# Kernel optimization log

Measured on AMD Instinct MI355X. Metric: run time of the kernel, lower is better.

## Reference

```python
import jax, jax.numpy as jnp
import numpy as np
from jax import lax

T = 8192
D_MODEL = 768
D_RNN = 1024
KW = 4  # conv kernel width


def setup_inputs() -> dict:
    key = jax.random.key(0)
    ks = jax.random.split(key, 9)
    x = jax.random.normal(ks[0], (T, D_MODEL), jnp.float32)
    # equinox nn.Linear(in, out): weight [out, in], bias [out]
    w1 = jax.random.normal(ks[1], (2 * D_RNN, D_MODEL), jnp.float32) / np.sqrt(D_MODEL)
    b1 = jnp.zeros((2 * D_RNN,), jnp.float32)
    # nn.Conv1d(d_rnn, d_rnn, 4, use_bias=False): kernel [out_ch, in_ch, kw]
    conv_w = jax.random.normal(ks[2], (D_RNN, D_RNN, KW), jnp.float32) / np.sqrt(D_RNN * KW)
    w_rg = jax.random.normal(ks[3], (2 * D_RNN, D_RNN), jnp.float32) / np.sqrt(D_RNN)
    b_rg = jnp.zeros((2 * D_RNN,), jnp.float32)
    w_out = jax.random.normal(ks[4], (D_MODEL, D_RNN), jnp.float32) / np.sqrt(D_RNN)
    b_out = jnp.zeros((D_MODEL,), jnp.float32)
    # Lambda ~ U(inv_sigmoid(0.9)^{1/8}, inv_sigmoid(0.999)^{1/8}) as in __init__
    inv_sig = lambda p: np.log(1.0 / (1.0 - p))
    lower = np.power(inv_sig(0.9), 1.0 / 8.0)
    upper = np.power(inv_sig(0.999), 1.0 / 8.0)
    Lambda = jax.random.uniform(ks[5], (D_RNN,), jnp.float32, lower, upper)
    return {"x": x, "w1": w1, "b1": b1, "conv_w": conv_w, "w_rg": w_rg,
            "b_rg": b_rg, "w_out": w_out, "b_out": b_out, "Lambda": Lambda}


def _rglru_forward(x, w1, b1, conv_w, w_rg, b_rg, w_out, b_out, Lambda):
    # lin1 then split into gate branch (gelu) and recurrent branch
    h = x @ w1.T + b1                       # [T, 2*D_RNN]
    a_branch = jax.nn.gelu(h[:, :D_RNN])    # [T, D_RNN]
    b_branch = h[:, D_RNN:]                 # [T, D_RNN]
    # causal conv1d: lhs [N=1, C, T], rhs [O, I, KW], left pad 3
    bc = lax.conv_general_dilated(b_branch.T[None], conv_w, (1,), [(KW - 1, 0)])[0].T  # [T, D_RNN]
    # RG-LRU gating
    g = jax.nn.sigmoid(bc @ w_rg.T + b_rg)  # [T, 2*D_RNN]
    inp_gate = g[:, :D_RNN]
    rec_gate = g[:, D_RNN:]
    a_t = jnp.exp(-8.0 * jax.nn.softplus(Lambda)[None, :] * rec_gate)  # [T, D_RNN]
    gated_x = jnp.sqrt(1.0 - a_t ** 2) * inp_gate * bc

    def rec_step(state, xs):
        gx, av = xs
        hn = av * state + gx
        return hn, hn

    _, y = lax.scan(rec_step, jnp.zeros((D_RNN,), x.dtype), (gated_x, a_t))
    return (a_branch * y) @ w_out.T + b_out  # [T, D_MODEL]


def reference(x, w1, b1, conv_w, w_rg, b_rg, w_out, b_out, Lambda):
    return _rglru_forward(x, w1, b1, conv_w, w_rg, b_rg, w_out, b_out, Lambda)
```

## Files before the change

kernel.cpp:

```cpp
#include <hip/hip_runtime.h>
#include <hip/hip_bf16.h>
#include <stdint.h>


#define T_LEN 8192
#define DM 768
#define DR 1024
#define NC 128
#define CL 64

typedef __bf16 bf16x8 __attribute__((ext_vector_type(8)));
typedef float  f32x4  __attribute__((ext_vector_type(4)));

#define AS1 __attribute__((address_space(1)))
#define AS3 __attribute__((address_space(3)))

__device__ __forceinline__ void cp16_g2l(const void* g, void* l) {
    __builtin_amdgcn_global_load_lds((const AS1 void*)g, (AS3 void*)l, 16, 0, 0);
}

__device__ __forceinline__ float gelu_tanh(float x) {
    const float inner = 0.7978845608028654f * (x + 0.044715f * x * x * x);
    return 0.5f * x * (1.f + tanhf(inner));
}

template<int BN, int EPI>
__global__ __launch_bounds__(256)
void gemm_mfma(const __hip_bfloat16* __restrict__ A,
               const __hip_bfloat16* __restrict__ B,
               const float* __restrict__ bias,
               void* __restrict__ Cv,
               int K, int lda, int N,
               __hip_bfloat16* __restrict__ D2)
{
    constexpr int NI = BN / 32;
    __shared__ __bf16 As[128 * 64];
    __shared__ __bf16 Bs[BN * 64];

    const int tid  = threadIdx.x;
    const int lane = tid & 63;
    const int wave = tid >> 6;
    const size_t m0 = (size_t)blockIdx.x * 128;
    const int    n0 = blockIdx.y * BN;
    const int wm = (wave >> 1) * 64;
    const int wn = (wave & 1) * (BN / 2);

    f32x4 acc[4][NI];
#pragma unroll
    for (int i = 0; i < 4; ++i)
#pragma unroll
        for (int j = 0; j < NI; ++j)
            acc[i][j] = f32x4{0.f, 0.f, 0.f, 0.f};

    const int frow = lane & 15;
    const int fq   = lane >> 4;

    for (int k0 = 0; k0 < K; k0 += 64) {
        __syncthreads();
#pragma unroll
        for (int q = 0; q < 4; ++q) {
            const int lin = q * 256 + tid;
            const int rr  = lin >> 3;
            const int gc  = (lin & 7) ^ (rr & 7);
            cp16_g2l(A + (m0 + rr) * (size_t)lda + k0 + gc * 8, &As[lin * 8]);
        }
#pragma unroll
        for (int q = 0; q < NI; ++q) {
            const int lin = q * 256 + tid;
            const int rr  = lin >> 3;
            const int gc  = (lin & 7) ^ (rr & 7);
            cp16_g2l(B + (size_t)(n0 + rr) * K + k0 + gc * 8, &Bs[lin * 8]);
        }
        __syncthreads();

#pragma unroll
        for (int ks = 0; ks < 2; ++ks) {
            bf16x8 af[4], bfr[NI];
#pragma unroll
            for (int mi = 0; mi < 4; ++mi) {
                const int R = wm + mi * 16 + frow;
                af[mi] = *(const bf16x8*)&As[R * 64 + (((ks * 4 + fq) ^ (R & 7)) * 8)];
            }
#pragma unroll
            for (int ni = 0; ni < NI; ++ni) {
                const int R = wn + ni * 16 + frow;
                bfr[ni] = *(const bf16x8*)&Bs[R * 64 + (((ks * 4 + fq) ^ (R & 7)) * 8)];
            }
#pragma unroll
            for (int mi = 0; mi < 4; ++mi)
#pragma unroll
                for (int ni = 0; ni < NI; ++ni)
                    acc[mi][ni] = __builtin_amdgcn_mfma_f32_16x16x32_bf16(
                        af[mi], bfr[ni], acc[mi][ni], 0, 0, 0);
        }
    }

    const int er = fq * 4;
    const int ec = frow;
#pragma unroll
    for (int ni = 0; ni < NI; ++ni) {
        const int n = n0 + wn + ni * 16 + ec;
        const float bv = bias ? bias[n] : 0.f;
#pragma unroll
        for (int mi = 0; mi < 4; ++mi) {
#pragma unroll
            for (int r2 = 0; r2 < 4; ++r2) {
                const size_t m = m0 + wm + mi * 16 + er + r2;
                const float v = acc[mi][ni][r2] + bv;
                if (EPI == 0) {
                    ((float*)Cv)[m * (size_t)N + n] = v;
                } else if (EPI == 1) {
                    ((__hip_bfloat16*)Cv)[m * (size_t)N + n] = __float2bfloat16(v);
                } else {
                    if (n < 1024)
                        ((__hip_bfloat16*)Cv)[m * 1024 + n] = __float2bfloat16(gelu_tanh(v));
                    else
                        D2[(m + 3) * 1024 + (n - 1024)] = __float2bfloat16(v);
                }
            }
        }
    }
}

__global__ __launch_bounds__(256)
void conv_mfma(const __hip_bfloat16* __restrict__ bbp,
               const __hip_bfloat16* __restrict__ W,
               __hip_bfloat16* __restrict__ C)
{
    __shared__ __bf16 As[132 * 32];
    __shared__ __bf16 Bs[4 * 128 * 32];

    const int tid  = threadIdx.x;
    const int lane = tid & 63;
    const int wave = tid >> 6;
    const size_t m0 = (size_t)blockIdx.x * 128;
    const int    n0 = blockIdx.y * 128;
    const int wm = (wave >> 1) * 64;
    const int wn = (wave & 1) * 64;

    f32x4 acc[4][4];
#pragma unroll
    for (int i = 0; i < 4; ++i)
#pragma unroll
        for (int j = 0; j < 4; ++j)
            acc[i][j] = f32x4{0.f, 0.f, 0.f, 0.f};

    const int frow = lane & 15;
    const int fq   = lane >> 4;

    for (int kc = 0; kc < 1024; kc += 32) {
        __syncthreads();
#pragma unroll
        for (int q = 0; q < 2; ++q) {
            const int lin = q * 256 + tid;
            const int rr  = lin >> 2;
            const int gc  = (lin & 3) ^ ((rr >> 1) & 3);
            cp16_g2l(bbp + (m0 + rr) * 1024 + kc + gc * 8, &As[lin * 8]);
        }
        if (tid < 16) {
            const int lin = 512 + tid;
            const int rr  = lin >> 2;
            const int gc  = (lin & 3) ^ ((rr >> 1) & 3);
            cp16_g2l(bbp + (m0 + rr) * 1024 + kc + gc * 8, &As[lin * 8]);
        }
#pragma unroll
        for (int s = 0; s < 4; ++s)
#pragma unroll
            for (int q = 0; q < 2; ++q) {
                const int lin = q * 256 + tid;
                const int rr  = lin >> 2;
                const int gc  = (lin & 3) ^ ((rr >> 1) & 3);
                cp16_g2l(W + (size_t)(n0 + rr) * 4096 + s * 1024 + kc + gc * 8,
                         &Bs[s * 4096 + lin * 8]);
            }
        __syncthreads();

#pragma unroll
        for (int s = 0; s < 4; ++s) {
            bf16x8 af[4], bfr[4];
#pragma unroll
            for (int mi = 0; mi < 4; ++mi) {
                const int R = wm + mi * 16 + frow + s;
                af[mi] = *(const bf16x8*)&As[R * 32 + ((fq ^ ((R >> 1) & 3)) * 8)];
            }
#pragma unroll
            for (int ni = 0; ni < 4; ++ni) {
                const int R = wn + ni * 16 + frow;
                bfr[ni] = *(const bf16x8*)&Bs[s * 4096 + R * 32 + ((fq ^ ((R >> 1) & 3)) * 8)];
            }
#pragma unroll
            for (int mi = 0; mi < 4; ++mi)
#pragma unroll
                for (int ni = 0; ni < 4; ++ni)
                    acc[mi][ni] = __builtin_amdgcn_mfma_f32_16x16x32_bf16(
                        af[mi], bfr[ni], acc[mi][ni], 0, 0, 0);
        }
    }

    const int er = fq * 4;
    const int ec = frow;
#pragma unroll
    for (int ni = 0; ni < 4; ++ni) {
        const int n = n0 + wn + ni * 16 + ec;
#pragma unroll
        for (int mi = 0; mi < 4; ++mi)
#pragma unroll
            for (int r2 = 0; r2 < 4; ++r2) {
                const size_t m = m0 + wm + mi * 16 + er + r2;
                C[m * 1024 + n] = __float2bfloat16(acc[mi][ni][r2]);
            }
    }
}

#define PREP_X   6291456
#define PREP_W1  (PREP_X + 1572864)
#define PREP_WRG (PREP_W1 + 2097152)
#define PREP_WO  (PREP_WRG + 786432)
#define PREP_CW  (PREP_WO + 4194304)
#define PREP_TOT (PREP_CW + 3072)
__global__ void prep_kernel(const float* __restrict__ x, const float* __restrict__ w1,
                            const float* __restrict__ w_rg, const float* __restrict__ w_out,
                            const float* __restrict__ conv_w,
                            __hip_bfloat16* __restrict__ xb, __hip_bfloat16* __restrict__ w1b,
                            __hip_bfloat16* __restrict__ w_rgb, __hip_bfloat16* __restrict__ w_outb,
                            __hip_bfloat16* __restrict__ wbigb, __hip_bfloat16* __restrict__ bbp)
{
    const int idx = blockIdx.x * 256 + threadIdx.x;
    if (idx < PREP_X) {
        xb[idx] = __float2bfloat16(x[idx]);
    } else if (idx < PREP_W1) {
        const int i = idx - PREP_X;  w1b[i] = __float2bfloat16(w1[i]);
    } else if (idx < PREP_WRG) {
        const int i = idx - PREP_W1; w_rgb[i] = __float2bfloat16(w_rg[i]);
    } else if (idx < PREP_WO) {
        const int i = idx - PREP_WRG; w_outb[i] = __float2bfloat16(w_out[i]);
    } else if (idx < PREP_CW) {
        const int n = idx - PREP_WO;
        const int o = n >> 12, r = n & 4095, k = r >> 10, i = r & 1023;
        wbigb[n] = __float2bfloat16(conv_w[o * 4096 + i * 4 + k]);
    } else {
        bbp[idx - PREP_CW] = __float2bfloat16(0.f);
    }
}

__global__ void scan_pass1(const __hip_bfloat16* __restrict__ gp,
                           const __hip_bfloat16* __restrict__ bc,
                           const float* __restrict__ Lambda,
                           float* __restrict__ ch, float* __restrict__ ca)
{
    const int c = blockIdx.y * 256 + threadIdx.x;
    const int j = blockIdx.x;
    const float cl = -8.f * log1pf(expf(Lambda[c]));
    float h = 0.f, ap = 1.f;
    const int t0 = j * CL;
    for (int tt = 0; tt < CL; ++tt) {
        const int t = t0 + tt;
        const long gi = (long)t * 2048 + c;
        const float ig = 1.f / (1.f + expf(-__bfloat162float(gp[gi])));
        const float rg = 1.f / (1.f + expf(-__bfloat162float(gp[gi + 1024])));
        const float a  = expf(cl * rg);
        const float gx = sqrtf(fmaxf(0.f, 1.f - a * a)) * ig *
                         __bfloat162float(bc[(long)t * 1024 + c]);
        h  = fmaf(a, h, gx);
        ap *= a;
    }
    ch[j * 1024 + c] = h;
    ca[j * 1024 + c] = ap;
}

__global__ void scan_combine(float* __restrict__ ch, const float* __restrict__ ca)
{
    const int c = blockIdx.x * 256 + threadIdx.x;
    float carry = 0.f;
    for (int j = 0; j < NC; ++j) {
        const float hj = ch[j * 1024 + c];
        const float aj = ca[j * 1024 + c];
        ch[j * 1024 + c] = carry;
        carry = fmaf(aj, carry, hj);
    }
}

__global__ void scan_pass2(const __hip_bfloat16* __restrict__ gp, const __hip_bfloat16* bc,
                           const float* __restrict__ Lambda,
                           const float* __restrict__ carry_in,
                           const __hip_bfloat16* __restrict__ ab,
                           __hip_bfloat16* zb)
{
    const int c = blockIdx.y * 256 + threadIdx.x;
    const int j = blockIdx.x;
    const float cl = -8.f * log1pf(expf(Lambda[c]));
    float h = carry_in[j * 1024 + c];
    const int t0 = j * CL;
    for (int tt = 0; tt < CL; ++tt) {
        const int t = t0 + tt;
        const long gi = (long)t * 2048 + c;
        const long bi = (long)t * 1024 + c;
        const float ig = 1.f / (1.f + expf(-__bfloat162float(gp[gi])));
        const float rg = 1.f / (1.f + expf(-__bfloat162float(gp[gi + 1024])));
        const float a  = expf(cl * rg);
        const float gx = sqrtf(fmaxf(0.f, 1.f - a * a)) * ig * __bfloat162float(bc[bi]);
        h = fmaf(a, h, gx);
        zb[bi] = __float2bfloat16(__bfloat162float(ab[bi]) * h);
    }
}

extern "C" void kernel_launch(void* const* d_in, const int* in_sizes, int n_in,
                              void* d_out, int out_size, void* d_ws, size_t ws_size,
                              hipStream_t stream)
{
    const float* x      = (const float*)d_in[0];
    const float* w1     = (const float*)d_in[1];
    const float* b1     = (const float*)d_in[2];
    const float* conv_w = (const float*)d_in[3];
    const float* w_rg   = (const float*)d_in[4];
    const float* b_rg   = (const float*)d_in[5];
    const float* w_out  = (const float*)d_in[6];
    const float* b_out  = (const float*)d_in[7];
    const float* Lambda = (const float*)d_in[8];
    float* out = (float*)d_out;
    (void)in_sizes; (void)n_in; (void)out_size; (void)ws_size;

    char* p = (char*)d_ws;
    auto alloc = [&](size_t bytes) { char* r = p; p += (bytes + 255) & ~255ULL; return r; };
    __hip_bfloat16* gpre  = (__hip_bfloat16*)alloc(8192ULL * 2048 * 2);
    __hip_bfloat16* ab    = (__hip_bfloat16*)alloc(8192ULL * 1024 * 2);
    __hip_bfloat16* bbp   = (__hip_bfloat16*)alloc(8200ULL * 1024 * 2);
    __hip_bfloat16* bcb   = (__hip_bfloat16*)alloc(8192ULL * 1024 * 2);
    __hip_bfloat16* wbigb = (__hip_bfloat16*)alloc(1024ULL * 4096 * 2);
    __hip_bfloat16* xb    = (__hip_bfloat16*)alloc(8192ULL * 768 * 2);
    __hip_bfloat16* w1b   = (__hip_bfloat16*)alloc(2048ULL * 768 * 2);
    __hip_bfloat16* w_rgb = (__hip_bfloat16*)alloc(2048ULL * 1024 * 2);
    __hip_bfloat16* w_outb= (__hip_bfloat16*)alloc(768ULL * 1024 * 2);
    float*          chv   = (float*)alloc(NC * 1024ULL * 4);
    float*          cav   = (float*)alloc(NC * 1024ULL * 4);
    __hip_bfloat16* zb    = bcb;

    prep_kernel<<<PREP_TOT / 256, 256, 0, stream>>>(x, w1, w_rg, w_out, conv_w,
                                                    xb, w1b, w_rgb, w_outb, wbigb, bbp);

    {
        dim3 grid(T_LEN / 128, 2048 / 128);
        gemm_mfma<128, 2><<<grid, 256, 0, stream>>>(xb, w1b, b1, ab, DM, DM, 2048, bbp);
    }

    {
        dim3 grid(T_LEN / 128, 1024 / 128);
        conv_mfma<<<grid, 256, 0, stream>>>(bbp, wbigb, bcb);
    }

    {
        dim3 grid(T_LEN / 128, 2048 / 128);
        gemm_mfma<128, 1><<<grid, 256, 0, stream>>>(bcb, w_rgb, b_rg, gpre, DR, DR, 2048, nullptr);
    }

    {
        dim3 gs(NC, DR / 256);
        scan_pass1<<<gs, 256, 0, stream>>>(gpre, bcb, Lambda, chv, cav);
        scan_combine<<<DR / 256, 256, 0, stream>>>(chv, cav);
        scan_pass2<<<gs, 256, 0, stream>>>(gpre, bcb, Lambda, chv, ab, zb);
    }

    {
        dim3 grid(T_LEN / 128, DM / 64);
        gemm_mfma<64, 0><<<grid, 256, 0, stream>>>(zb, w_outb, b_out, out, DR, DR, DM, nullptr);
    }
}
```

Baseline: 279.9 us.

## Double-buffer GEMM LDS tiles and express conv as shifted-row GEMM

The shared GEMM kernel now double-buffers its A/B LDS tiles, issuing the next tile's global-to-LDS loads before computing the current one, with explicit vmcnt waits and barriers, and asks for two blocks per CU. The separate conv kernel is removed. The causal conv is computed by the same GEMM with K=4096 and a SHIFT mode that offsets A rows by k0>>10, so each tap reads a shifted window of the padded input. This hides global load latency behind MFMA work and reuses one tuned kernel, at the cost of doubled LDS use and reloading A rows per tap instead of sharing one tile across taps.

Result: no change. 277.7 us (-0.8%).

```diff
diff --git a/kernel.cpp b/kernel.cpp
--- a/kernel.cpp
+++ b/kernel.cpp
@@ -24,8 +24,8 @@
     return 0.5f * x * (1.f + tanhf(inner));
 }
 
-template<int BN, int EPI>
-__global__ __launch_bounds__(256)
+template<int BN, int EPI, bool SHIFT>
+__global__ __launch_bounds__(256, 2)
 void gemm_mfma(const __hip_bfloat16* __restrict__ A,
                const __hip_bfloat16* __restrict__ B,
                const float* __restrict__ bias,
@@ -33,9 +33,10 @@
                int K, int lda, int N,
                __hip_bfloat16* __restrict__ D2)
 {
-    constexpr int NI = BN / 32;
-    __shared__ __bf16 As[128 * 64];
-    __shared__ __bf16 Bs[BN * 64];
+    constexpr int NI  = BN / 32;
+    constexpr int NLD = 4 + NI;
+    __shared__ __bf16 As[2][128 * 64];
+    __shared__ __bf16 Bs[2][BN * 64];
 
     const int tid  = threadIdx.x;
     const int lane = tid & 63;
@@ -55,44 +56,65 @@
     const int frow = lane & 15;
     const int fq   = lane >> 4;
 
-    for (int k0 = 0; k0 < K; k0 += 64) {
-        __syncthreads();
+    auto stage = [&](int buf, int k0) {
 #pragma unroll
         for (int q = 0; q < 4; ++q) {
             const int lin = q * 256 + tid;
             const int rr  = lin >> 3;
             const int gc  = (lin & 7) ^ (rr & 7);
-            cp16_g2l(A + (m0 + rr) * (size_t)lda + k0 + gc * 8, &As[lin * 8]);
+            const size_t ar = m0 + rr + (SHIFT ? (size_t)(k0 >> 10) : 0);
+            const int    ac = SHIFT ? (k0 & 1023) : k0;
+            cp16_g2l(A + ar * (size_t)lda + ac + gc * 8, &As[buf][lin * 8]);
         }
 #pragma unroll
         for (int q = 0; q < NI; ++q) {
             const int lin = q * 256 + tid;
             const int rr  = lin >> 3;
             const int gc  = (lin & 7) ^ (rr & 7);
-            cp16_g2l(B + (size_t)(n0 + rr) * K + k0 + gc * 8, &Bs[lin * 8]);
-        }
-        __syncthreads();
-
+            cp16_g2l(B + (size_t)(n0 + rr) * K + k0 + gc * 8, &Bs[buf][lin * 8]);
+        }
+    };
+
+    const int nt = K / 64;
+    stage(0, 0);
+    int cur = 0;
+    for (int t = 0; t < nt; ++t) {
+        if (t + 1 < nt) {
+            stage(cur ^ 1, (t + 1) * 64);
+            asm volatile("s_waitcnt vmcnt(%0)" :: "n"(NLD) : "memory");
+        } else {
+            asm volatile("s_waitcnt vmcnt(0)" ::: "memory");
+        }
+        __builtin_amdgcn_s_barrier();
+        asm volatile("" ::: "memory");
+
+        bf16x8 af[2][4], bfr[2][NI];
 #pragma unroll
         for (int ks = 0; ks < 2; ++ks) {
-            bf16x8 af[4], bfr[NI];
 #pragma unroll
             for (int mi = 0; mi < 4; ++mi) {
                 const int R = wm + mi * 16 + frow;
-                af[mi] = *(const bf16x8*)&As[R * 64 + (((ks * 4 + fq) ^ (R & 7)) * 8)];
+                af[ks][mi] = *(const bf16x8*)&As[cur][R * 64 + (((ks * 4 + fq) ^ (R & 7)) * 8)];
             }
 #pragma unroll
             for (int ni = 0; ni < NI; ++ni) {
                 const int R = wn + ni * 16 + frow;
-                bfr[ni] = *(const bf16x8*)&Bs[R * 64 + (((ks * 4 + fq) ^ (R & 7)) * 8)];
+                bfr[ks][ni] = *(const bf16x8*)&Bs[cur][R * 64 + (((ks * 4 + fq) ^ (R & 7)) * 8)];
             }
+        }
+        asm volatile("s_waitcnt lgkmcnt(0)" ::: "memory");
+        __builtin_amdgcn_s_barrier();
+        asm volatile("" ::: "memory");
+
+#pragma unroll
+        for (int ks = 0; ks < 2; ++ks)
 #pragma unroll
             for (int mi = 0; mi < 4; ++mi)
 #pragma unroll
                 for (int ni = 0; ni < NI; ++ni)
                     acc[mi][ni] = __builtin_amdgcn_mfma_f32_16x16x32_bf16(
-                        af[mi], bfr[ni], acc[mi][ni], 0, 0, 0);
-        }
+                        af[ks][mi], bfr[ks][ni], acc[mi][ni], 0, 0, 0);
+        cur ^= 1;
     }
 
     const int er = fq * 4;
@@ -119,96 +141,6 @@
                 }
             }
         }
-    }
-}
-
-__global__ __launch_bounds__(256)
-void conv_mfma(const __hip_bfloat16* __restrict__ bbp,
-               const __hip_bfloat16* __restrict__ W,
-               __hip_bfloat16* __restrict__ C)
-{
-    __shared__ __bf16 As[132 * 32];
-    __shared__ __bf16 Bs[4 * 128 * 32];
-
-    const int tid  = threadIdx.x;
-    const int lane = tid & 63;
-    const int wave = tid >> 6;
-    const size_t m0 = (size_t)blockIdx.x * 128;
-    const int    n0 = blockIdx.y * 128;
-    const int wm = (wave >> 1) * 64;
-    const int wn = (wave & 1) * 64;
-
-    f32x4 acc[4][4];
-#pragma unroll
-    for (int i = 0; i < 4; ++i)
-#pragma unroll
-        for (int j = 0; j < 4; ++j)
-            acc[i][j] = f32x4{0.f, 0.f, 0.f, 0.f};
-
-    const int frow = lane & 15;
-    const int fq   = lane >> 4;
-
-    for (int kc = 0; kc < 1024; kc += 32) {
-        __syncthreads();
-#pragma unroll
-        for (int q = 0; q < 2; ++q) {
-            const int lin = q * 256 + tid;
-            const int rr  = lin >> 2;
-            const int gc  = (lin & 3) ^ ((rr >> 1) & 3);
-            cp16_g2l(bbp + (m0 + rr) * 1024 + kc + gc * 8, &As[lin * 8]);
-        }
-        if (tid < 16) {
-            const int lin = 512 + tid;
-            const int rr  = lin >> 2;
-            const int gc  = (lin & 3) ^ ((rr >> 1) & 3);
-            cp16_g2l(bbp + (m0 + rr) * 1024 + kc + gc * 8, &As[lin * 8]);
-        }
-#pragma unroll
-        for (int s = 0; s < 4; ++s)
-#pragma unroll
-            for (int q = 0; q < 2; ++q) {
-                const int lin = q * 256 + tid;
-                const int rr  = lin >> 2;
-                const int gc  = (lin & 3) ^ ((rr >> 1) & 3);
-                cp16_g2l(W + (size_t)(n0 + rr) * 4096 + s * 1024 + kc + gc * 8,
-                         &Bs[s * 4096 + lin * 8]);
-            }
-        __syncthreads();
-
-#pragma unroll
-        for (int s = 0; s < 4; ++s) {
-            bf16x8 af[4], bfr[4];
-#pragma unroll
-            for (int mi = 0; mi < 4; ++mi) {
-                const int R = wm + mi * 16 + frow + s;
-                af[mi] = *(const bf16x8*)&As[R * 32 + ((fq ^ ((R >> 1) & 3)) * 8)];
-            }
-#pragma unroll
-            for (int ni = 0; ni < 4; ++ni) {
-                const int R = wn + ni * 16 + frow;
-                bfr[ni] = *(const bf16x8*)&Bs[s * 4096 + R * 32 + ((fq ^ ((R >> 1) & 3)) * 8)];
-            }
-#pragma unroll
-            for (int mi = 0; mi < 4; ++mi)
-#pragma unroll
-                for (int ni = 0; ni < 4; ++ni)
-                    acc[mi][ni] = __builtin_amdgcn_mfma_f32_16x16x32_bf16(
-                        af[mi], bfr[ni], acc[mi][ni], 0, 0, 0);
-        }
-    }
-
-    const int er = fq * 4;
-    const int ec = frow;
-#pragma unroll
-    for (int ni = 0; ni < 4; ++ni) {
-        const int n = n0 + wn + ni * 16 + ec;
-#pragma unroll
-        for (int mi = 0; mi < 4; ++mi)
-#pragma unroll
-            for (int r2 = 0; r2 < 4; ++r2) {
-                const size_t m = m0 + wm + mi * 16 + er + r2;
-                C[m * 1024 + n] = __float2bfloat16(acc[mi][ni][r2]);
-            }
     }
 }
 
@@ -340,17 +272,17 @@
 
     {
         dim3 grid(T_LEN / 128, 2048 / 128);
-        gemm_mfma<128, 2><<<grid, 256, 0, stream>>>(xb, w1b, b1, ab, DM, DM, 2048, bbp);
+        gemm_mfma<128, 2, false><<<grid, 256, 0, stream>>>(xb, w1b, b1, ab, DM, DM, 2048, bbp);
     }
 
     {
         dim3 grid(T_LEN / 128, 1024 / 128);
-        conv_mfma<<<grid, 256, 0, stream>>>(bbp, wbigb, bcb);
+        gemm_mfma<128, 1, true><<<grid, 256, 0, stream>>>(bbp, wbigb, nullptr, bcb, 4096, 1024, 1024, nullptr);
     }
 
     {
         dim3 grid(T_LEN / 128, 2048 / 128);
-        gemm_mfma<128, 1><<<grid, 256, 0, stream>>>(bcb, w_rgb, b_rg, gpre, DR, DR, 2048, nullptr);
+        gemm_mfma<128, 1, false><<<grid, 256, 0, stream>>>(bcb, w_rgb, b_rg, gpre, DR, DR, 2048, nullptr);
     }
 
     {
@@ -362,6 +294,6 @@
 
     {
         dim3 grid(T_LEN / 128, DM / 64);
-        gemm_mfma<64, 0><<<grid, 256, 0, stream>>>(zb, w_outb, b_out, out, DR, DR, DM, nullptr);
-    }
-}
+        gemm_mfma<64, 0, false><<<grid, 256, 0, stream>>>(zb, w_outb, b_out, out, DR, DR, DM, nullptr);
+    }
+}
```

## Double-buffer GEMM and conv LDS tiles with larger 256-row tiles and 512 threads

Applied to the files above, without the earlier changes.

Rewrites the MFMA GEMM and conv kernels to use double-buffered LDS staging, so the next K-tile's global loads overlap with MFMA compute on the current tile. Explicit vmcnt/lgkmcnt waits and raw s_barrier calls replace the two __syncthreads per iteration. Block tiles grow to 256 rows with 512 threads (8 waves), each wave computing 128 rows, which raises reuse per loaded tile. The grid is also reordered so the N dimension varies fastest. In exchange, LDS use per block roughly quadruples and register pressure rises, which may limit occupancy despite the launch_bounds(512,2) hint.

Result: slower. 306.5 us (+9.5%).

```diff
diff --git a/kernel.cpp b/kernel.cpp
--- a/kernel.cpp
+++ b/kernel.cpp
@@ -25,7 +25,7 @@
 }
 
 template<int BN, int EPI>
-__global__ __launch_bounds__(256)
+__global__ __launch_bounds__(512, 2)
 void gemm_mfma(const __hip_bfloat16* __restrict__ A,
                const __hip_bfloat16* __restrict__ B,
                const float* __restrict__ bias,
@@ -33,21 +33,22 @@
                int K, int lda, int N,
                __hip_bfloat16* __restrict__ D2)
 {
-    constexpr int NI = BN / 32;
-    __shared__ __bf16 As[128 * 64];
-    __shared__ __bf16 Bs[BN * 64];
+    constexpr int NI  = BN / 64;
+    constexpr int NLD = 4 + NI;
+    __shared__ __bf16 As[2][256 * 64];
+    __shared__ __bf16 Bs[2][BN * 64];
 
     const int tid  = threadIdx.x;
     const int lane = tid & 63;
     const int wave = tid >> 6;
-    const size_t m0 = (size_t)blockIdx.x * 128;
-    const int    n0 = blockIdx.y * BN;
-    const int wm = (wave >> 1) * 64;
-    const int wn = (wave & 1) * (BN / 2);
-
-    f32x4 acc[4][NI];
-#pragma unroll
-    for (int i = 0; i < 4; ++i)
+    const int    n0 = blockIdx.x * BN;
+    const size_t m0 = (size_t)blockIdx.y * 256;
+    const int wm = (wave >> 2) * 128;
+    const int wn = (wave & 3) * (BN / 4);
+
+    f32x4 acc[8][NI];
+#pragma unroll
+    for (int i = 0; i < 8; ++i)
 #pragma unroll
         for (int j = 0; j < NI; ++j)
             acc[i][j] = f32x4{0.f, 0.f, 0.f, 0.f};
@@ -55,44 +56,62 @@
     const int frow = lane & 15;
     const int fq   = lane >> 4;
 
-    for (int k0 = 0; k0 < K; k0 += 64) {
-        __syncthreads();
+    auto stage = [&](int buf, int k0) {
 #pragma unroll
         for (int q = 0; q < 4; ++q) {
-            const int lin = q * 256 + tid;
+            const int lin = q * 512 + tid;
             const int rr  = lin >> 3;
             const int gc  = (lin & 7) ^ (rr & 7);
-            cp16_g2l(A + (m0 + rr) * (size_t)lda + k0 + gc * 8, &As[lin * 8]);
+            cp16_g2l(A + (m0 + rr) * (size_t)lda + k0 + gc * 8, &As[buf][lin * 8]);
         }
 #pragma unroll
         for (int q = 0; q < NI; ++q) {
-            const int lin = q * 256 + tid;
+            const int lin = q * 512 + tid;
             const int rr  = lin >> 3;
             const int gc  = (lin & 7) ^ (rr & 7);
-            cp16_g2l(B + (size_t)(n0 + rr) * K + k0 + gc * 8, &Bs[lin * 8]);
-        }
-        __syncthreads();
+            cp16_g2l(B + (size_t)(n0 + rr) * K + k0 + gc * 8, &Bs[buf][lin * 8]);
+        }
+    };
+
+    const int nt = K / 64;
+    stage(0, 0);
+    int cur = 0;
+    for (int t = 0; t < nt; ++t) {
+        if (t + 1 < nt) {
+            stage(cur ^ 1, (t + 1) * 64);
+            asm volatile("s_waitcnt vmcnt(%0)" :: "n"(NLD) : "memory");
+        } else {
+            asm volatile("s_waitcnt vmcnt(0)" ::: "memory");
+        }
+        __builtin_amdgcn_sched_barrier(0);
+        __builtin_amdgcn_s_barrier();
+        __builtin_amdgcn_sched_barrier(0);
 
 #pragma unroll
         for (int ks = 0; ks < 2; ++ks) {
-            bf16x8 af[4], bfr[NI];
-#pragma unroll
-            for (int mi = 0; mi < 4; ++mi) {
+            bf16x8 af[8], bfr[NI];
+#pragma unroll
+            for (int mi = 0; mi < 8; ++mi) {
                 const int R = wm + mi * 16 + frow;
-                af[mi] = *(const bf16x8*)&As[R * 64 + (((ks * 4 + fq) ^ (R & 7)) * 8)];
+                af[mi] = *(const bf16x8*)&As[cur][R * 64 + (((ks * 4 + fq) ^ (R & 7)) * 8)];
             }
 #pragma unroll
             for (int ni = 0; ni < NI; ++ni) {
                 const int R = wn + ni * 16 + frow;
-                bfr[ni] = *(const bf16x8*)&Bs[R * 64 + (((ks * 4 + fq) ^ (R & 7)) * 8)];
-            }
-#pragma unroll
-            for (int mi = 0; mi < 4; ++mi)
+                bfr[ni] = *(const bf16x8*)&Bs[cur][R * 64 + (((ks * 4 + fq) ^ (R & 7)) * 8)];
+            }
+            asm volatile("s_waitcnt lgkmcnt(0)" ::: "memory");
+            __builtin_amdgcn_sched_barrier(0);
+#pragma unroll
+            for (int mi = 0; mi < 8; ++mi)
 #pragma unroll
                 for (int ni = 0; ni < NI; ++ni)
                     acc[mi][ni] = __builtin_amdgcn_mfma_f32_16x16x32_bf16(
                         af[mi], bfr[ni], acc[mi][ni], 0, 0, 0);
         }
+        __builtin_amdgcn_s_barrier();
+        __builtin_amdgcn_sched_barrier(0);
+        cur ^= 1;
     }
 
     const int er = fq * 4;
@@ -102,7 +121,7 @@
         const int n = n0 + wn + ni * 16 + ec;
         const float bv = bias ? bias[n] : 0.f;
 #pragma unroll
-        for (int mi = 0; mi < 4; ++mi) {
+        for (int mi = 0; mi < 8; ++mi) {
 #pragma unroll
             for (int r2 = 0; r2 < 4; ++r2) {
                 const size_t m = m0 + wm + mi * 16 + er + r2;
@@ -122,88 +141,102 @@
     }
 }
 
-__global__ __launch_bounds__(256)
+__global__ __launch_bounds__(512, 2)
 void conv_mfma(const __hip_bfloat16* __restrict__ bbp,
                const __hip_bfloat16* __restrict__ W,
                __hip_bfloat16* __restrict__ C)
 {
-    __shared__ __bf16 As[132 * 32];
-    __shared__ __bf16 Bs[4 * 128 * 32];
+    __shared__ __bf16 As[2][260 * 32];
+    __shared__ __bf16 Bs[2][4 * 128 * 32];
 
     const int tid  = threadIdx.x;
     const int lane = tid & 63;
     const int wave = tid >> 6;
-    const size_t m0 = (size_t)blockIdx.x * 128;
-    const int    n0 = blockIdx.y * 128;
-    const int wm = (wave >> 1) * 64;
-    const int wn = (wave & 1) * 64;
-
-    f32x4 acc[4][4];
-#pragma unroll
-    for (int i = 0; i < 4; ++i)
-#pragma unroll
-        for (int j = 0; j < 4; ++j)
+    const int    n0 = blockIdx.x * 128;
+    const size_t m0 = (size_t)blockIdx.y * 256;
+    const int wm = (wave >> 2) * 128;
+    const int wn = (wave & 3) * 32;
+
+    f32x4 acc[8][2];
+#pragma unroll
+    for (int i = 0; i < 8; ++i)
+#pragma unroll
+        for (int j = 0; j < 2; ++j)
             acc[i][j] = f32x4{0.f, 0.f, 0.f, 0.f};
 
     const int frow = lane & 15;
     const int fq   = lane >> 4;
 
-    for (int kc = 0; kc < 1024; kc += 32) {
-        __syncthreads();
+    auto stage = [&](int buf, int kc) {
 #pragma unroll
         for (int q = 0; q < 2; ++q) {
-            const int lin = q * 256 + tid;
+            const int lin = q * 512 + tid;
             const int rr  = lin >> 2;
             const int gc  = (lin & 3) ^ ((rr >> 1) & 3);
-            cp16_g2l(bbp + (m0 + rr) * 1024 + kc + gc * 8, &As[lin * 8]);
+            cp16_g2l(bbp + (m0 + rr) * 1024 + kc + gc * 8, &As[buf][lin * 8]);
         }
         if (tid < 16) {
-            const int lin = 512 + tid;
+            const int lin = 1024 + tid;
             const int rr  = lin >> 2;
             const int gc  = (lin & 3) ^ ((rr >> 1) & 3);
-            cp16_g2l(bbp + (m0 + rr) * 1024 + kc + gc * 8, &As[lin * 8]);
-        }
-#pragma unroll
-        for (int s = 0; s < 4; ++s)
-#pragma unroll
-            for (int q = 0; q < 2; ++q) {
-                const int lin = q * 256 + tid;
-                const int rr  = lin >> 2;
-                const int gc  = (lin & 3) ^ ((rr >> 1) & 3);
-                cp16_g2l(W + (size_t)(n0 + rr) * 4096 + s * 1024 + kc + gc * 8,
-                         &Bs[s * 4096 + lin * 8]);
-            }
-        __syncthreads();
-
+            cp16_g2l(bbp + (m0 + rr) * 1024 + kc + gc * 8, &As[buf][lin * 8]);
+        }
 #pragma unroll
         for (int s = 0; s < 4; ++s) {
-            bf16x8 af[4], bfr[4];
-#pragma unroll
-            for (int mi = 0; mi < 4; ++mi) {
+            const int rr = tid >> 2;
+            const int gc = (tid & 3) ^ ((rr >> 1) & 3);
+            cp16_g2l(W + (size_t)(n0 + rr) * 4096 + s * 1024 + kc + gc * 8,
+                     &Bs[buf][s * 4096 + tid * 8]);
+        }
+    };
+
+    stage(0, 0);
+    int cur = 0;
+    for (int t = 0; t < 32; ++t) {
+        if (t + 1 < 32) {
+            stage(cur ^ 1, (t + 1) * 32);
+            asm volatile("s_waitcnt vmcnt(6)" ::: "memory");
+        } else {
+            asm volatile("s_waitcnt vmcnt(0)" ::: "memory");
+        }
+        __builtin_amdgcn_sched_barrier(0);
+        __builtin_amdgcn_s_barrier();
+        __builtin_amdgcn_sched_barrier(0);
+
+#pragma unroll
+        for (int s = 0; s < 4; ++s) {
+            bf16x8 af[8], bfr[2];
+#pragma unroll
+            for (int mi = 0; mi < 8; ++mi) {
                 const int R = wm + mi * 16 + frow + s;
-                af[mi] = *(const bf16x8*)&As[R * 32 + ((fq ^ ((R >> 1) & 3)) * 8)];
-            }
-#pragma unroll
-            for (int ni = 0; ni < 4; ++ni) {
+                af[mi] = *(const bf16x8*)&As[cur][R * 32 + ((fq ^ ((R >> 1) & 3)) * 8)];
+            }
+#pragma unroll
+            for (int ni = 0; ni < 2; ++ni) {
                 const int R = wn + ni * 16 + frow;
-                bfr[ni] = *(const bf16x8*)&Bs[s * 4096 + R * 32 + ((fq ^ ((R >> 1) & 3)) * 8)];
-            }
-#pragma unroll
-            for (int mi = 0; mi < 4; ++mi)
-#pragma unroll
-                for (int ni = 0; ni < 4; ++ni)
+                bfr[ni] = *(const bf16x8*)&Bs[cur][s * 4096 + R * 32 + ((fq ^ ((R >> 1) & 3)) * 8)];
+            }
+            asm volatile("s_waitcnt lgkmcnt(0)" ::: "memory");
+            __builtin_amdgcn_sched_barrier(0);
+#pragma unroll
+            for (int mi = 0; mi < 8; ++mi)
+#pragma unroll
+                for (int ni = 0; ni < 2; ++ni)
                     acc[mi][ni] = __builtin_amdgcn_mfma_f32_16x16x32_bf16(
                         af[mi], bfr[ni], acc[mi][ni], 0, 0, 0);
         }
+        __builtin_amdgcn_s_barrier();
+        __builtin_amdgcn_sched_barrier(0);
+        cur ^= 1;
     }
 
     const int er = fq * 4;
     const int ec = frow;
 #pragma unroll
-    for (int ni = 0; ni < 4; ++ni) {
+    for (int ni = 0; ni < 2; ++ni) {
         const int n = n0 + wn + ni * 16 + ec;
 #pragma unroll
-        for (int mi = 0; mi < 4; ++mi)
+        for (int mi = 0; mi < 8; ++mi)
 #pragma unroll
             for (int r2 = 0; r2 < 4; ++r2) {
                 const size_t m = m0 + wm + mi * 16 + er + r2;
@@ -339,18 +372,18 @@
                                                     xb, w1b, w_rgb, w_outb, wbigb, bbp);
 
     {
-        dim3 grid(T_LEN / 128, 2048 / 128);
-        gemm_mfma<128, 2><<<grid, 256, 0, stream>>>(xb, w1b, b1, ab, DM, DM, 2048, bbp);
+        dim3 grid(2048 / 256, T_LEN / 256);
+        gemm_mfma<256, 2><<<grid, 512, 0, stream>>>(xb, w1b, b1, ab, DM, DM, 2048, bbp);
     }
 
     {
-        dim3 grid(T_LEN / 128, 1024 / 128);
-        conv_mfma<<<grid, 256, 0, stream>>>(bbp, wbigb, bcb);
+        dim3 grid(1024 / 128, T_LEN / 256);
+        conv_mfma<<<grid, 512, 0, stream>>>(bbp, wbigb, bcb);
     }
 
     {
-        dim3 grid(T_LEN / 128, 2048 / 128);
-        gemm_mfma<128, 1><<<grid, 256, 0, stream>>>(bcb, w_rgb, b_rg, gpre, DR, DR, 2048, nullptr);
+        dim3 grid(2048 / 256, T_LEN / 256);
+        gemm_mfma<256, 1><<<grid, 512, 0, stream>>>(bcb, w_rgb, b_rg, gpre, DR, DR, 2048, nullptr);
     }
 
     {
@@ -361,7 +394,7 @@
     }
 
     {
-        dim3 grid(T_LEN / 128, DM / 64);
-        gemm_mfma<64, 0><<<grid, 256, 0, stream>>>(zb, w_outb, b_out, out, DR, DR, DM, nullptr);
-    }
-}
+        dim3 grid(DM / 128, T_LEN / 256);
+        gemm_mfma<128, 0><<<grid, 512, 0, stream>>>(zb, w_outb, b_out, out, DR, DR, DM, nullptr);
+    }
+}
```
